# Performance work log

Hardware: AMD Instinct MI355X
Metric: run time of the kernel (lower is better)

The kernel has to match this reference:

```python
import jax, jax.numpy as jnp
import numpy as np
from jax import lax

ALPHA = 1.5
N_ITER = 100


def entmax(z, alpha=ALPHA, n_iter=N_ITER):
    # z: [B, Sq, Sk] scores. Bisection for the entmax threshold tau.
    z = (alpha - 1.0) * z.astype(jnp.float32)
    S = z.shape[-1]
    z_max = jnp.max(z, axis=-1, keepdims=True)          # [B, Sq, 1]
    tau_min = z_max - 1.0
    tau_max = z_max - np.float32(S ** (1.0 - alpha))
    inv = 1.0 / (alpha - 1.0)                            # = 2.0 for alpha=1.5

    def body(carry, _):
        tmin, tmax, _ = carry
        tau = (tmin + tmax) * 0.5
        p = jnp.maximum(z - tau, 0.0) ** inv             # [B, Sq, Sk]
        Z = jnp.sum(p, axis=-1, keepdims=True)           # [B, Sq, 1]
        tmin = jnp.where(Z >= 1.0, tau, tmin)
        tmax = jnp.where(Z < 1.0, tau, tmax)
        return (tmin, tmax, tau), None

    init = (tau_min, tau_max, (tau_min + tau_max) * 0.5)
    (tmin, tmax, tau), _ = lax.scan(jax.checkpoint(body), init, None, length=n_iter)
    # faithful to the TF code: final output uses p, Z from the LAST iteration's tau
    p = jnp.maximum(z - tau, 0.0) ** inv
    Z = jnp.sum(p, axis=-1, keepdims=True)
    return p / Z


def setup_inputs() -> dict:
    key = jax.random.key(0)
    kq, kk, kv = jax.random.split(key, 3)
    B, S, D = 8, 2048, 128
    return {
        "query": jax.random.normal(kq, (B, S, D), dtype=jnp.float32),
        "key": jax.random.normal(kk, (B, S, D), dtype=jnp.float32),
        "value": jax.random.normal(kv, (B, S, D), dtype=jnp.float32),
    }


def reference(query, key, value):
    scores = jnp.einsum("bqd,bkd->bqk", query, key)      # QK^T, no scaling (as in source)
    weights = entmax(scores, alpha=ALPHA, n_iter=N_ITER)
    return jnp.einsum("bqk,bkd->bqd", weights, value)
```

## Files before the change

kernel.cpp:

```cpp
#include <hip/hip_runtime.h>

#define BB 8
#define SS 2048
#define DD 128
#define ROWS 16
#define NW 8
#define CTW 16

typedef short bf16x8 __attribute__((ext_vector_type(8)));
typedef float f32x4 __attribute__((ext_vector_type(4)));

template <int I> struct IC { static constexpr int value = I; };
template <int I, int N, typename F>
__device__ __forceinline__ void sfor(F&& f) {
  if constexpr (I < N) { f(IC<I>{}); sfor<I + 1, N>((F&&)f); }
}

__device__ __forceinline__ short f2bf(float x) {
  return __builtin_bit_cast(short, (__bf16)x);
}

__device__ __forceinline__ void stage_tile(const short* g, short* l) {
#pragma unroll
  for (int s = 0; s < 4; ++s) {
    __builtin_amdgcn_global_load_lds(
        (const __attribute__((address_space(1))) void*)(g + (s << 9)),
        (__attribute__((address_space(3))) void*)(l + (s << 9)), 16, 0, 0);
  }
}

__global__ __launch_bounds__(256)
void ksplit(const float* __restrict__ K, short* __restrict__ Khi) {
  const int lin = blockIdx.x * 256 + threadIdx.x;
  const int r   = lin >> 4;
  const int c8  = lin & 15;
  const float4 v0 = *(const float4*)(K + (size_t)lin * 8);
  const float4 v1 = *(const float4*)(K + (size_t)lin * 8 + 4);
  bf16x8 h;
  h[0] = f2bf(v0.x); h[1] = f2bf(v0.y); h[2] = f2bf(v0.z); h[3] = f2bf(v0.w);
  h[4] = f2bf(v1.x); h[5] = f2bf(v1.y); h[6] = f2bf(v1.z); h[7] = f2bf(v1.w);
  const int bct  = r >> 4;
  const int m16  = r & 15;
  const int s    = c8 >> 2;
  const int quad = c8 & 3;
  const size_t out = ((((size_t)bct * 4 + s) * 64) + quad * 16 + m16) * 8;
  *(bf16x8*)(Khi + out) = h;
}

__global__ __launch_bounds__(512) __attribute__((amdgpu_waves_per_eu(3, 4)))
void attn(const float* __restrict__ Q, const short* __restrict__ Khi,
          const float* __restrict__ K, const float* __restrict__ V,
          float* __restrict__ Out) {
  __shared__ short kring[NW][2][2048];
  __shared__ unsigned short Qs[ROWS][136];
  __shared__ float rbuf[ROWS][64];
  __shared__ int   scol[ROWS][64];
  __shared__ float exM[NW][ROWS];
  __shared__ int   rcnt[ROWS];
  __shared__ int   rovf[ROWS];
  __shared__ float tauB[ROWS], ZB[ROWS];

  const int tid  = threadIdx.x;
  const int lane = tid & 63;
  const int wid  = __builtin_amdgcn_readfirstlane(tid >> 6);
  const int quad = lane >> 4, m16 = lane & 15;
  const int b    = blockIdx.x & 7;
  const int qt   = blockIdx.x >> 3;

  const float* Qb = Q + (size_t)(b * SS + qt * ROWS) * DD;
  const float* Kb = K + (size_t)b * SS * DD;
  const float* Vb = V + (size_t)b * SS * DD;
  float*       Ob = Out + (size_t)(b * SS + qt * ROWS) * DD;
  const short* KHb = Khi + (size_t)b * SS * DD;

  if (tid < ROWS) { rcnt[tid] = 0; rovf[tid] = 0; }

  {
    const int row = tid >> 5, d = (tid & 31) * 4;
    const float4 v = *(const float4*)&Qb[row * DD + d];
    ushort4 h;
    h.x = (unsigned short)f2bf(0.5f * v.x);
    h.y = (unsigned short)f2bf(0.5f * v.y);
    h.z = (unsigned short)f2bf(0.5f * v.z);
    h.w = (unsigned short)f2bf(0.5f * v.w);
    *(ushort4*)&Qs[row][d] = h;
  }
  __syncthreads();

  bf16x8 qh[4];
#pragma unroll
  for (int s = 0; s < 4; ++s)
    qh[s] = *(const bf16x8*)&Qs[m16][s * 32 + quad * 8];

  short* ring0 = &kring[wid][0][0];
  short* ring1 = &kring[wid][1][0];
  const short* gw = KHb + ((size_t)(wid * CTW) << 11) + lane * 8;

  stage_tile(gw + 0 * 2048, ring0);
  stage_tile(gw + 1 * 2048, ring1);

  f32x4 acc[CTW];
  sfor<0, CTW>([&](auto ic) {
    constexpr int i = ic.value;
    if constexpr (i < CTW - 1) asm volatile("s_waitcnt vmcnt(4)" ::: "memory");
    else                       asm volatile("s_waitcnt vmcnt(0)" ::: "memory");
    const short* sbl = ((i & 1) ? ring1 : ring0) + lane * 8;
    f32x4 c = {0.f, 0.f, 0.f, 0.f};
    sfor<0, 4>([&](auto sc) {
      constexpr int s = sc.value;
      const bf16x8 bh = *(const bf16x8*)(sbl + (s << 9));
      c = __builtin_amdgcn_mfma_f32_16x16x32_bf16(qh[s], bh, c, 0, 0, 0);
    });
    acc[i] = c;
    if constexpr (i + 2 < CTW) {
      asm volatile("s_waitcnt lgkmcnt(0)" ::: "memory");
      stage_tile(gw + (i + 2) * 2048, (i & 1) ? ring1 : ring0);
    }
  });

  float mx[4] = {-1e38f, -1e38f, -1e38f, -1e38f};
  sfor<0, CTW>([&](auto ic) {
#pragma unroll
    for (int j = 0; j < 4; ++j) mx[j] = fmaxf(mx[j], acc[ic.value][j]);
  });
#pragma unroll
  for (int j = 0; j < 4; ++j)
#pragma unroll
    for (int s = 1; s <= 8; s <<= 1) mx[j] = fmaxf(mx[j], __shfl_xor(mx[j], s));
  if (m16 == 0) {
#pragma unroll
    for (int j = 0; j < 4; ++j) exM[wid][4 * quad + j] = mx[j];
  }
  __syncthreads();
  float M4[4];
#pragma unroll
  for (int j = 0; j < 4; ++j) {
    float m = -1e38f;
#pragma unroll
    for (int w = 0; w < NW; ++w) m = fmaxf(m, exM[w][4 * quad + j]);
    M4[j] = m;
  }

  sfor<0, CTW>([&](auto ic) {
    constexpr int i = ic.value;
    const int col = wid * 256 + i * 16 + m16;
#pragma unroll
    for (int j = 0; j < 4; ++j) {
      const int row = 4 * quad + j;
      if (acc[i][j] > M4[j] - 1.25f) {
        const int pos = atomicAdd(&rcnt[row], 1);
        if (pos < 64) { scol[row][pos] = col; rbuf[row][pos] = acc[i][j]; }
        else rovf[row] = 1;
      }
    }
  });
  __syncthreads();

  const int rr32 = lane >> 5;
  const int row  = 2 * wid + rr32;
  const int l32  = lane & 31;
  const int nA = rcnt[2 * wid]     < 64 ? rcnt[2 * wid]     : 64;
  const int nB = rcnt[2 * wid + 1] < 64 ? rcnt[2 * wid + 1] : 64;
  const int nr  = rr32 ? nB : nA;
  const int nmx = nA > nB ? nA : nB;

  {
    const float4 q4 = *(const float4*)&Qb[row * DD + l32 * 4];
    for (int i = 0; i < nmx; ++i) {
      const bool act = i < nr;
      const int c = act ? scol[row][i] : scol[row][0];
      const float4 k4 = *(const float4*)&Kb[(size_t)c * DD + l32 * 4];
      float t = q4.x * k4.x + q4.y * k4.y + q4.z * k4.z + q4.w * k4.w;
#pragma unroll
      for (int s = 1; s <= 16; s <<= 1) t += __shfl_xor(t, s);
      if (act && l32 == 0) rbuf[row][i] = 0.5f * t;
    }
  }

  {
    const float a0 = (l32 < nr)      ? rbuf[row][l32]      : -1e38f;
    const float a1 = (l32 + 32 < nr) ? rbuf[row][l32 + 32] : -1e38f;
    float Mr = fmaxf(a0, a1);
#pragma unroll
    for (int s = 1; s <= 16; s <<= 1) Mr = fmaxf(Mr, __shfl_xor(Mr, s));
    float tmn = Mr - 1.0f, tmx = Mr - 0.022097086912079608f;
    float tau = 0.5f * (tmn + tmx), Zr = 0.f;
    for (int it = 0; it < 100; ++it) {
      tau = 0.5f * (tmn + tmx);
      const float t0 = fmaxf(a0 - tau, 0.f);
      const float t1 = fmaxf(a1 - tau, 0.f);
      float zp = fmaf(t0, t0, t1 * t1);
#pragma unroll
      for (int s = 1; s <= 16; s <<= 1) zp += __shfl_xor(zp, s);
      Zr = zp;
      const float nmn = (zp >= 1.f) ? tau : tmn;
      const float nmx2 = (zp >= 1.f) ? tmx : tau;
      const bool ch = (nmn != tmn) || (nmx2 != tmx);
      tmn = nmn; tmx = nmx2;
      if (!__any(ch)) break;
    }
    if (l32 == 0) { tauB[row] = tau; ZB[row] = Zr; }
  }

  if (!rovf[row]) {
    const float tau = tauB[row];
    const float iz  = 1.0f / ZB[row];
    float4 o = {0.f, 0.f, 0.f, 0.f};
    for (int i = 0; i < nr; ++i) {
      const float rv = rbuf[row][i];
      const float tt = fmaxf(rv - tau, 0.f);
      const float pi = tt * tt * iz;
      const int   c  = scol[row][i];
      const float4 v4 = *(const float4*)&Vb[(size_t)c * DD + l32 * 4];
      o.x = fmaf(pi, v4.x, o.x);
      o.y = fmaf(pi, v4.y, o.y);
      o.z = fmaf(pi, v4.z, o.z);
      o.w = fmaf(pi, v4.w, o.w);
    }
    *(float4*)&Ob[row * DD + l32 * 4] = o;
  }

#pragma unroll
  for (int rr = 0; rr < 2; ++rr) {
    const int frow = 2 * wid + rr;
    if (!rovf[frow]) continue;
    float* zr = (float*)&kring[wid][0][0];
    for (int c0 = 0; c0 < 32; ++c0) {
      const int c = c0 * 64 + lane;
      const float* kp = &Kb[(size_t)c * DD];
      float t = 0.f;
      for (int d = 0; d < DD; d += 4) {
        const float4 qv = *(const float4*)&Qb[frow * DD + d];
        const float4 kv = *(const float4*)&kp[d];
        t = fmaf(qv.x, kv.x, t); t = fmaf(qv.y, kv.y, t);
        t = fmaf(qv.z, kv.z, t); t = fmaf(qv.w, kv.w, t);
      }
      zr[c] = 0.5f * t;
    }
    float Mr = -1e38f;
    for (int c0 = 0; c0 < 32; ++c0) Mr = fmaxf(Mr, zr[c0 * 64 + lane]);
#pragma unroll
    for (int s = 1; s <= 32; s <<= 1) Mr = fmaxf(Mr, __shfl_xor(Mr, s));
    float tmn = Mr - 1.0f, tmx = Mr - 0.022097086912079608f;
    float tau = 0.5f * (tmn + tmx), Zr = 0.f;
    for (int it = 0; it < 100; ++it) {
      tau = 0.5f * (tmn + tmx);
      float zp = 0.f;
      for (int c0 = 0; c0 < 32; ++c0) {
        const float tt = fmaxf(zr[c0 * 64 + lane] - tau, 0.f);
        zp = fmaf(tt, tt, zp);
      }
#pragma unroll
      for (int s = 1; s <= 32; s <<= 1) zp += __shfl_xor(zp, s);
      Zr = zp;
      const float nmn = (zp >= 1.f) ? tau : tmn;
      const float nmx2 = (zp >= 1.f) ? tmx : tau;
      const bool ch = (nmn != tmn) || (nmx2 != tmx);
      tmn = nmn; tmx = nmx2;
      if (!__any(ch)) break;
    }
    const float iz = 1.0f / Zr;
    float2 o = {0.f, 0.f};
    for (int c = 0; c < SS; ++c) {
      const float tt = fmaxf(zr[c] - tau, 0.f);
      if (tt > 0.f) {
        const float pi = tt * tt * iz;
        const float2 v2 = *(const float2*)&Vb[(size_t)c * DD + lane * 2];
        o.x = fmaf(pi, v2.x, o.x);
        o.y = fmaf(pi, v2.y, o.y);
      }
    }
    *(float2*)&Ob[frow * DD + lane * 2] = o;
  }
}

extern "C" void kernel_launch(void* const* d_in, const int* in_sizes, int n_in,
                              void* d_out, int out_size, void* d_ws, size_t ws_size,
                              hipStream_t stream) {
  const float* Q = (const float*)d_in[0];
  const float* K = (const float*)d_in[1];
  const float* V = (const float*)d_in[2];
  float* out = (float*)d_out;
  short* Khi = (short*)d_ws;

  hipLaunchKernelGGL(ksplit, dim3(BB * SS * DD / (256 * 8)), dim3(256), 0, stream,
                     K, Khi);
  hipLaunchKernelGGL(attn, dim3(BB * (SS / ROWS)), dim3(512), 0, stream,
                     Q, Khi, K, V, out);
}
```

Measured before the change: 127.2 us.

## Replace bisection threshold search with exact sort-free closed-form entmax tau

Swaps the up-to-100-step bisection for the alpha=1.5 threshold for an exact closed form. Each lane takes its candidate values as the support boundary, builds the support count, sum and sum of squares over the row, and solves the quadratic for tau. Valid candidates are then picked with a wave max reduction. This removes the serial iteration and its shuffle reductions per step in exchange for an O(n) loop over the candidate list per lane. It also changes numerics relative to the bisection reference, which stops at floating-point convergence.

```diff
diff --git a/kernel.cpp b/kernel.cpp
--- a/kernel.cpp
+++ b/kernel.cpp
@@ -178,28 +178,44 @@
   }
 
   {
-    const float a0 = (l32 < nr)      ? rbuf[row][l32]      : -1e38f;
-    const float a1 = (l32 + 32 < nr) ? rbuf[row][l32 + 32] : -1e38f;
-    float Mr = fmaxf(a0, a1);
-#pragma unroll
-    for (int s = 1; s <= 16; s <<= 1) Mr = fmaxf(Mr, __shfl_xor(Mr, s));
-    float tmn = Mr - 1.0f, tmx = Mr - 0.022097086912079608f;
-    float tau = 0.5f * (tmn + tmx), Zr = 0.f;
-    for (int it = 0; it < 100; ++it) {
-      tau = 0.5f * (tmn + tmx);
-      const float t0 = fmaxf(a0 - tau, 0.f);
-      const float t1 = fmaxf(a1 - tau, 0.f);
-      float zp = fmaf(t0, t0, t1 * t1);
-#pragma unroll
-      for (int s = 1; s <= 16; s <<= 1) zp += __shfl_xor(zp, s);
-      Zr = zp;
-      const float nmn = (zp >= 1.f) ? tau : tmn;
-      const float nmx2 = (zp >= 1.f) ? tmx : tau;
-      const bool ch = (nmn != tmn) || (nmx2 != tmx);
-      tmn = nmn; tmx = nmx2;
-      if (!__any(ch)) break;
-    }
-    if (l32 == 0) { tauB[row] = tau; ZB[row] = Zr; }
+    const float z0 = (l32 < nr)      ? rbuf[row][l32]      : -1e38f;
+    const float z1 = (l32 + 32 < nr) ? rbuf[row][l32 + 32] : -1e38f;
+    float k0 = 0.f, S10 = 0.f, S20 = 0.f, nb0 = -1e38f;
+    float k1 = 0.f, S11 = 0.f, S21 = 0.f, nb1 = -1e38f;
+    for (int j = 0; j < nr; ++j) {
+      const float w = rbuf[row][j];
+      const bool ge0 = (w > z0) || (w == z0 && j <= l32);
+      k0  += ge0 ? 1.f : 0.f;
+      S10 += ge0 ? w : 0.f;
+      S20  = ge0 ? fmaf(w, w, S20) : S20;
+      nb0  = (!ge0 && w > nb0) ? w : nb0;
+      const bool ge1 = (w > z1) || (w == z1 && j <= l32 + 32);
+      k1  += ge1 ? 1.f : 0.f;
+      S11 += ge1 ? w : 0.f;
+      S21  = ge1 ? fmaf(w, w, S21) : S21;
+      nb1  = (!ge1 && w > nb1) ? w : nb1;
+    }
+    const float d0 = fmaxf(fmaf(S10, S10, -k0 * (S20 - 1.f)), 0.f);
+    const float d1 = fmaxf(fmaf(S11, S11, -k1 * (S21 - 1.f)), 0.f);
+    const float tau0 = (S10 - __builtin_sqrtf(d0)) / fmaxf(k0, 1.f);
+    const float tau1 = (S11 - __builtin_sqrtf(d1)) / fmaxf(k1, 1.f);
+    const bool v0b = z0 > tau0, v1b = z1 > tau1;
+    const bool v0  = v0b && (nb0 <= tau0);
+    const bool v1  = v1b && (nb1 <= tau1);
+    float tv = fmaxf(v0 ? tau0 : -1e38f, v1 ? tau1 : -1e38f);
+    float tb = fmaxf(v0b ? tau0 : -1e38f, v1b ? tau1 : -1e38f);
+#pragma unroll
+    for (int s = 1; s <= 16; s <<= 1) {
+      tv = fmaxf(tv, __shfl_xor(tv, s));
+      tb = fmaxf(tb, __shfl_xor(tb, s));
+    }
+    const float tau = (tv > -1e37f) ? tv : tb;
+    const float p0 = fmaxf(z0 - tau, 0.f);
+    const float p1 = fmaxf(z1 - tau, 0.f);
+    float zp = fmaf(p0, p0, p1 * p1);
+#pragma unroll
+    for (int s = 1; s <= 16; s <<= 1) zp += __shfl_xor(zp, s);
+    if (l32 == 0) { tauB[row] = tau; ZB[row] = zp; }
   }
 
   if (!rovf[row]) {
```

After: 117.0 us (median of 2 runs). 8.0% less time.
